# Kernel tuning notes

Hardware: AMD Instinct MI355X
Metric: run time of the kernel (lower is better)

## Reference

```python
import jax, jax.numpy as jnp
import numpy as np

N, NFEAT, NHID, NCLASS = 8192, 512, 256, 16
ALPHA = 0.01          # LeakyReLU negative slope
NEG = -9.0e15         # mask fill value from the original code
ADJ_DENSITY = 0.01    # ~82 neighbors per node


def setup_inputs() -> dict:
    key = jax.random.key(0)
    ks = jax.random.split(key, 9)
    x = jax.random.normal(ks[0], (N, NFEAT), jnp.float32)
    # sparse binary adjacency with self-loops, stored dense as in the torch code
    adj = (jax.random.uniform(ks[1], (N, N)) < ADJ_DENSITY).astype(jnp.int32)
    adj = adj.at[jnp.arange(N), jnp.arange(N)].set(1)
    s = 0.05
    W1 = jax.random.normal(ks[2], (NFEAT, NHID), jnp.float32) * s   # gc1.weight
    b1 = jax.random.normal(ks[3], (NHID,), jnp.float32) * s         # gc1.bias
    Wa = jax.random.normal(ks[4], (NHID, NHID), jnp.float32) * s    # out_att.W (nhid*nheads -> nhid)
    a_vec = jax.random.normal(ks[5], (2 * NHID, 1), jnp.float32) * s  # out_att.a
    W3 = jax.random.normal(ks[6], (NHID, NCLASS), jnp.float32) * s  # gc3.weight
    b3 = jax.random.normal(ks[7], (NCLASS,), jnp.float32) * s       # gc3.bias
    return {"x": x, "adj": adj, "W1": W1, "b1": b1, "Wa": Wa,
            "a_vec": a_vec, "W3": W3, "b3": b3}


def reference(x, adj, W1, b1, Wa, a_vec, W3, b3):
    adjf = adj.astype(x.dtype)
    # gc1: spmm(adj, x @ W1) + b1, then ReLU  (eval mode -> dropout is identity)
    h1 = jax.nn.relu(adjf @ (x @ W1) + b1)        # [N, NHID]
    feat = h1
    # out_att (GraphAttentionLayer, concat=False)
    Wh = h1 @ Wa                                   # [N, NHID]
    f1 = Wh @ a_vec[:NHID]                         # [N, 1]
    f2 = Wh @ a_vec[NHID:]                         # [N, 1]
    e = jax.nn.leaky_relu(f1 + f2.T, ALPHA)        # dense [N, N] scores
    e = jnp.where(adj > 0, e, jnp.asarray(NEG, x.dtype))
    attention = jax.nn.softmax(e, axis=1)          # row-wise masked softmax
    h_prime = attention @ Wh                       # [N, NHID]
    a_out = jax.nn.elu(h_prime)                    # x = F.elu(a)
    # gc3
    out = adjf @ (a_out @ W3) + b3                 # [N, NCLASS]
    return (jax.nn.sigmoid(out), attention, jnp.concatenate([feat, out], axis=1))
```

## Files before the change

kernel.cpp:

```cpp
#include <hip/hip_runtime.h>
#include <hip/hip_bf16.h>

#define NN    8192
#define NFEAT 512
#define NHID  256
#define NCLASS 16
#define ELLW  256

typedef __hip_bfloat16 bf16;
typedef unsigned short u16;
typedef __bf16 bf16x8 __attribute__((ext_vector_type(8)));
typedef float  f32x4  __attribute__((ext_vector_type(4)));
typedef int    i32x4  __attribute__((ext_vector_type(4)));

__global__ __launch_bounds__(256) void probe_dtype2(const u16* __restrict__ a, int na,
                                                    const u16* __restrict__ b, int nb,
                                                    int* __restrict__ cnt) {
  int c = 0;
  for (int i = blockIdx.x * 256 + threadIdx.x; i < na; i += gridDim.x * 256)
    if (((a[i] >> 7) & 0xFF) == 0xFF) c++;
  for (int i = blockIdx.x * 256 + threadIdx.x; i < nb; i += gridDim.x * 256)
    if (((b[i] >> 7) & 0xFF) == 0xFF) c++;
  if (c) atomicAdd(cnt, c);
}

__global__ __launch_bounds__(256) void convert_bf(const void* __restrict__ src,
                                                  bf16* __restrict__ dst, int n,
                                                  const int* __restrict__ flagcnt) {
  bool isf32 = (*flagcnt > 16);
  int i = blockIdx.x * 256 + threadIdx.x;
  if (i < n) {
    if (isf32) dst[i] = __float2bfloat16(((const float*)src)[i]);
    else       dst[i] = ((const bf16*)src)[i];
  }
}

__global__ __launch_bounds__(256) void convert_rest(const void* __restrict__ W1r,
                                                    const void* __restrict__ War,
                                                    const void* __restrict__ b1r,
                                                    const void* __restrict__ avr,
                                                    const void* __restrict__ W3r,
                                                    const void* __restrict__ b3r,
                                                    bf16* __restrict__ W1t,
                                                    bf16* __restrict__ Wat,
                                                    float* __restrict__ b1f,
                                                    float* __restrict__ avecf,
                                                    float* __restrict__ W3f,
                                                    float* __restrict__ b3f,
                                                    const int* __restrict__ flagcnt) {
  bool isf32 = (*flagcnt > 16);
  auto rd = [&](const void* p, int i) -> float {
    return isf32 ? ((const float*)p)[i] : __bfloat162float(((const bf16*)p)[i]);
  };
  const int n1 = NFEAT * NHID;
  const int n2 = n1 + NHID * NHID;
  const int n3 = n2 + NHID;
  const int n4 = n3 + 2 * NHID;
  const int n5 = n4 + NHID * NCLASS;
  const int n6 = n5 + NCLASS;
  for (int i = blockIdx.x * 256 + threadIdx.x; i < n6; i += gridDim.x * 256) {
    if (i < n1)      { int k = i / NHID, n = i % NHID; W1t[(size_t)n * NFEAT + k] = __float2bfloat16(rd(W1r, i)); }
    else if (i < n2) { int j = i - n1; int k = j / NHID, n = j % NHID; Wat[(size_t)n * NHID + k] = __float2bfloat16(rd(War, j)); }
    else if (i < n3) b1f[i - n2] = rd(b1r, i - n2);
    else if (i < n4) avecf[i - n3] = rd(avr, i - n3);
    else if (i < n5) W3f[i - n4] = rd(W3r, i - n4);
    else             b3f[i - n5] = rd(b3r, i - n5);
  }
}

__global__ __launch_bounds__(256) void build_ell(const int* __restrict__ adj,
                                                 int* __restrict__ ell_cnt,
                                                 u16* __restrict__ ell_col) {
  __shared__ int cnt;
  int row = blockIdx.x;
  if (threadIdx.x == 0) cnt = 0;
  __syncthreads();
  const i32x4* arow = (const i32x4*)(adj + (size_t)row * NN);
  u16* crow = ell_col + (size_t)row * ELLW;
  int lane = threadIdx.x & 63;
  unsigned long long lt = ((unsigned long long)1 << lane) - 1;
  for (int j4 = threadIdx.x; j4 < NN / 4; j4 += 256) {
    i32x4 v = __builtin_nontemporal_load(&arow[j4]);
    unsigned long long m0 = __ballot(v.x != 0);
    unsigned long long m1 = __ballot(v.y != 0);
    unsigned long long m2 = __ballot(v.z != 0);
    unsigned long long m3 = __ballot(v.w != 0);
    int c0 = __popcll(m0), c1 = __popcll(m1), c2 = __popcll(m2), c3 = __popcll(m3);
    int total = c0 + c1 + c2 + c3;
    int base = 0;
    if (lane == 0 && total) base = atomicAdd(&cnt, total);
    base = __shfl(base, 0, 64);
    int col = j4 * 4;
    if (v.x) { int p = base + __popcll(m0 & lt);                 if (p < ELLW) crow[p] = (u16)col;       }
    if (v.y) { int p = base + c0 + __popcll(m1 & lt);            if (p < ELLW) crow[p] = (u16)(col + 1); }
    if (v.z) { int p = base + c0 + c1 + __popcll(m2 & lt);       if (p < ELLW) crow[p] = (u16)(col + 2); }
    if (v.w) { int p = base + c0 + c1 + c2 + __popcll(m3 & lt);  if (p < ELLW) crow[p] = (u16)(col + 3); }
  }
  __syncthreads();
  if (threadIdx.x == 0) ell_cnt[row] = cnt < ELLW ? cnt : ELLW;
}

#define TM 64
#define TN 64
#define LDSP 72

__global__ __launch_bounds__(256) void gemm_bt(const bf16* __restrict__ A, int lda,
                                               const bf16* __restrict__ Bt, int ldb,
                                               bf16* __restrict__ C, int ldc, int K) {
  __shared__ __align__(16) bf16 sA[TM * LDSP];
  __shared__ __align__(16) bf16 sB[TN * LDSP];
  int bm = blockIdx.x, bn = blockIdx.y;
  int t = threadIdx.x;
  int wave = t >> 6, lane = t & 63;
  int quad = lane >> 4, l16 = lane & 15;
  f32x4 acc[4] = {};

  int srow = t >> 2;
  int sk   = (t & 3) * 16;
  const size_t abase = (size_t)(bm * TM + srow) * lda + sk;
  const size_t bbase = (size_t)(bn * TN + srow) * ldb + sk;

  uint4 pa0 = *(const uint4*)&A[abase];
  uint4 pa1 = *(const uint4*)&A[abase + 8];
  uint4 pb0 = *(const uint4*)&Bt[bbase];
  uint4 pb1 = *(const uint4*)&Bt[bbase + 8];

  for (int kt = 0; kt < K; kt += 64) {
    *(uint4*)&sA[srow * LDSP + sk]     = pa0;
    *(uint4*)&sA[srow * LDSP + sk + 8] = pa1;
    *(uint4*)&sB[srow * LDSP + sk]     = pb0;
    *(uint4*)&sB[srow * LDSP + sk + 8] = pb1;
    __syncthreads();
    if (kt + 64 < K) {
      pa0 = *(const uint4*)&A[abase + kt + 64];
      pa1 = *(const uint4*)&A[abase + kt + 72];
      pb0 = *(const uint4*)&Bt[bbase + kt + 64];
      pb1 = *(const uint4*)&Bt[bbase + kt + 72];
    }
    bf16x8 af0 = *(const bf16x8*)&sA[(wave * 16 + l16) * LDSP + quad * 8];
    bf16x8 af1 = *(const bf16x8*)&sA[(wave * 16 + l16) * LDSP + 32 + quad * 8];
#pragma unroll
    for (int c = 0; c < 4; ++c) {
      bf16x8 bf0 = *(const bf16x8*)&sB[(c * 16 + l16) * LDSP + quad * 8];
      bf16x8 bf1 = *(const bf16x8*)&sB[(c * 16 + l16) * LDSP + 32 + quad * 8];
      acc[c] = __builtin_amdgcn_mfma_f32_16x16x32_bf16(af0, bf0, acc[c], 0, 0, 0);
      acc[c] = __builtin_amdgcn_mfma_f32_16x16x32_bf16(af1, bf1, acc[c], 0, 0, 0);
    }
    __syncthreads();
  }
  int row0 = bm * TM + wave * 16 + quad * 4;
  int col0 = bn * TN;
#pragma unroll
  for (int c = 0; c < 4; ++c) {
#pragma unroll
    for (int r = 0; r < 4; ++r) {
      C[(size_t)(row0 + r) * ldc + col0 + c * 16 + l16] = __float2bfloat16(acc[c][r]);
    }
  }
}

__global__ __launch_bounds__(256) void spmm_h1(const bf16* __restrict__ XW,
                                               const int* __restrict__ ell_cnt,
                                               const u16* __restrict__ ell_col,
                                               const float* __restrict__ b1,
                                               float* __restrict__ out2,
                                               bf16* __restrict__ h1b) {
  __shared__ int sc0[ELLW], sc1[ELLW];
  int r0 = blockIdx.x * 2, r1 = r0 + 1;
  int t = threadIdx.x;
  int nn0 = ell_cnt[r0], nn1 = ell_cnt[r1];
  const u16* c0 = ell_col + (size_t)r0 * ELLW;
  const u16* c1 = ell_col + (size_t)r1 * ELLW;
  for (int k = t; k < nn0; k += 256) sc0[k] = c0[k];
  for (int k = t; k < nn1; k += 256) sc1[k] = c1[k];
  __syncthreads();
  float a0 = 0.f, a1 = 0.f;
#pragma unroll 4
  for (int k = 0; k < nn0; ++k) a0 += __bfloat162float(XW[(size_t)sc0[k] * NHID + t]);
#pragma unroll 4
  for (int k = 0; k < nn1; ++k) a1 += __bfloat162float(XW[(size_t)sc1[k] * NHID + t]);
  float bb = b1[t];
  a0 = fmaxf(a0 + bb, 0.f);
  a1 = fmaxf(a1 + bb, 0.f);
  out2[(size_t)r0 * (NHID + NCLASS) + t] = a0;
  out2[(size_t)r1 * (NHID + NCLASS) + t] = a1;
  h1b[(size_t)r0 * NHID + t] = __float2bfloat16(a0);
  h1b[(size_t)r1 * NHID + t] = __float2bfloat16(a1);
}

__global__ __launch_bounds__(256) void f12_kernel(const bf16* __restrict__ Wh,
                                                  const float* __restrict__ avec,
                                                  float* __restrict__ f12) {
  int wave = threadIdx.x >> 6, lane = threadIdx.x & 63;
  int row = blockIdx.x * 4 + wave;
  const bf16* wr = Wh + (size_t)row * NHID;
  float s1 = 0.f, s2 = 0.f;
  for (int k = lane; k < NHID; k += 64) {
    float w = __bfloat162float(wr[k]);
    s1 += w * avec[k];
    s2 += w * avec[NHID + k];
  }
  for (int o = 32; o > 0; o >>= 1) {
    s1 += __shfl_down(s1, o, 64);
    s2 += __shfl_down(s2, o, 64);
  }
  if (lane == 0) { f12[row] = s1; f12[NN + row] = s2; }
}

__global__ __launch_bounds__(256) void attn_fused(const bf16* __restrict__ Wh,
                                                  const int* __restrict__ ell_cnt,
                                                  const u16* __restrict__ ell_col,
                                                  const float* __restrict__ f12,
                                                  float* __restrict__ att,
                                                  bf16* __restrict__ aout) {
  __shared__ float p[ELLW];
  __shared__ int scols[ELLW];
  __shared__ float red[8];
  int row = blockIdx.x, t = threadIdx.x;
  int nn = ell_cnt[row];
  const u16* cr = ell_col + (size_t)row * ELLW;
  float f1i = f12[row];
  const float* f2 = f12 + NN;

  f32x4* dst = (f32x4*)(att + (size_t)row * NN);
  f32x4 z = {0.f, 0.f, 0.f, 0.f};
#pragma unroll
  for (int k = t; k < NN / 4; k += 256) __builtin_nontemporal_store(z, &dst[k]);

  for (int k = t; k < nn; k += 256) scols[k] = cr[k];
  __syncthreads();

  float lmax = -1e30f;
  for (int k = t; k < nn; k += 256) {
    float e = f1i + f2[scols[k]];
    e = (e > 0.f) ? e : 0.01f * e;
    p[k] = e;
    lmax = fmaxf(lmax, e);
  }
  for (int o = 32; o > 0; o >>= 1) lmax = fmaxf(lmax, __shfl_down(lmax, o, 64));
  if ((t & 63) == 0) red[t >> 6] = lmax;
  __syncthreads();
  float gmax = fmaxf(fmaxf(red[0], red[1]), fmaxf(red[2], red[3]));

  float lsum = 0.f;
  for (int k = t; k < nn; k += 256) {
    float ex = __expf(p[k] - gmax);
    p[k] = ex;
    lsum += ex;
  }
  for (int o = 32; o > 0; o >>= 1) lsum += __shfl_down(lsum, o, 64);
  __syncthreads();
  if ((t & 63) == 0) red[4 + (t >> 6)] = lsum;
  __syncthreads();
  float inv = 1.f / fmaxf(red[4] + red[5] + red[6] + red[7], 1e-30f);

  for (int k = t; k < nn; k += 256)
    att[(size_t)row * NN + scols[k]] = p[k] * inv;

  float acc = 0.f;
#pragma unroll 8
  for (int k = 0; k < nn; ++k)
    acc += p[k] * __bfloat162float(Wh[(size_t)scols[k] * NHID + t]);
  acc *= inv;
  float e = (acc > 0.f) ? acc : (__expf(acc) - 1.f);
  aout[(size_t)row * NHID + t] = __float2bfloat16(e);
}

__global__ __launch_bounds__(256) void attn_sparse(const bf16* __restrict__ Wh,
                                                   const int* __restrict__ ell_cnt,
                                                   const u16* __restrict__ ell_col,
                                                   const float* __restrict__ f12,
                                                   bf16* __restrict__ aout) {
  __shared__ float p[ELLW];
  __shared__ int scols[ELLW];
  __shared__ float red[8];
  int row = blockIdx.x, t = threadIdx.x;
  int nn = ell_cnt[row];
  const u16* cr = ell_col + (size_t)row * ELLW;
  float f1i = f12[row];
  const float* f2 = f12 + NN;
  for (int k = t; k < nn; k += 256) scols[k] = cr[k];
  __syncthreads();
  float lmax = -1e30f;
  for (int k = t; k < nn; k += 256) {
    float e = f1i + f2[scols[k]];
    e = (e > 0.f) ? e : 0.01f * e;
    p[k] = e;
    lmax = fmaxf(lmax, e);
  }
  for (int o = 32; o > 0; o >>= 1) lmax = fmaxf(lmax, __shfl_down(lmax, o, 64));
  if ((t & 63) == 0) red[t >> 6] = lmax;
  __syncthreads();
  float gmax = fmaxf(fmaxf(red[0], red[1]), fmaxf(red[2], red[3]));
  float lsum = 0.f;
  for (int k = t; k < nn; k += 256) {
    float ex = __expf(p[k] - gmax);
    p[k] = ex;
    lsum += ex;
  }
  for (int o = 32; o > 0; o >>= 1) lsum += __shfl_down(lsum, o, 64);
  __syncthreads();
  if ((t & 63) == 0) red[4 + (t >> 6)] = lsum;
  __syncthreads();
  float inv = 1.f / fmaxf(red[4] + red[5] + red[6] + red[7], 1e-30f);
  float acc = 0.f;
  for (int k = 0; k < nn; ++k)
    acc += p[k] * __bfloat162float(Wh[(size_t)scols[k] * NHID + t]);
  acc *= inv;
  float e = (acc > 0.f) ? acc : (__expf(acc) - 1.f);
  aout[(size_t)row * NHID + t] = __float2bfloat16(e);
}

__global__ __launch_bounds__(256) void attn_dense(const int* __restrict__ adj,
                                                  const float* __restrict__ f12,
                                                  float* __restrict__ att) {
  __shared__ __align__(16) float rowbuf[NN];
  __shared__ float se[ELLW];
  __shared__ int sj[ELLW];
  __shared__ float red[8];
  __shared__ int cnt;
  int row = blockIdx.x, t = threadIdx.x;
  if (t == 0) cnt = 0;
  f32x4* rb4 = (f32x4*)rowbuf;
  f32x4 z = {0.f, 0.f, 0.f, 0.f};
  for (int k = t; k < NN / 4; k += 256) rb4[k] = z;
  float f1i = f12[row];
  const float* f2 = f12 + NN;
  __syncthreads();
  const int4* arow = (const int4*)(adj + (size_t)row * NN);
  for (int j4 = t; j4 < NN / 4; j4 += 256) {
    int4 v = arow[j4];
    int base = j4 * 4;
    if (v.x) { int p = atomicAdd(&cnt, 1); if (p < ELLW) { sj[p] = base;     se[p] = f1i + f2[base];     } }
    if (v.y) { int p = atomicAdd(&cnt, 1); if (p < ELLW) { sj[p] = base + 1; se[p] = f1i + f2[base + 1]; } }
    if (v.z) { int p = atomicAdd(&cnt, 1); if (p < ELLW) { sj[p] = base + 2; se[p] = f1i + f2[base + 2]; } }
    if (v.w) { int p = atomicAdd(&cnt, 1); if (p < ELLW) { sj[p] = base + 3; se[p] = f1i + f2[base + 3]; } }
  }
  __syncthreads();
  int nn = cnt < ELLW ? cnt : ELLW;
  float lmax = -1e30f;
  for (int k = t; k < nn; k += 256) {
    float e = se[k];
    e = (e > 0.f) ? e : 0.01f * e;
    se[k] = e;
    lmax = fmaxf(lmax, e);
  }
  for (int o = 32; o > 0; o >>= 1) lmax = fmaxf(lmax, __shfl_down(lmax, o, 64));
  if ((t & 63) == 0) red[t >> 6] = lmax;
  __syncthreads();
  float gmax = fmaxf(fmaxf(red[0], red[1]), fmaxf(red[2], red[3]));
  float lsum = 0.f;
  for (int k = t; k < nn; k += 256) {
    float ex = __expf(se[k] - gmax);
    se[k] = ex;
    lsum += ex;
  }
  for (int o = 32; o > 0; o >>= 1) lsum += __shfl_down(lsum, o, 64);
  __syncthreads();
  if ((t & 63) == 0) red[4 + (t >> 6)] = lsum;
  __syncthreads();
  float inv = 1.f / fmaxf(red[4] + red[5] + red[6] + red[7], 1e-30f);
  for (int k = t; k < nn; k += 256) rowbuf[sj[k]] = se[k] * inv;
  __syncthreads();
  const f32x4* src = (const f32x4*)rowbuf;
  f32x4* dst = (f32x4*)(att + (size_t)row * NN);
  for (int k = t; k < NN / 4; k += 256) dst[k] = src[k];
}

__global__ __launch_bounds__(256) void gemm3(const bf16* __restrict__ aout,
                                             const float* __restrict__ W3,
                                             float* __restrict__ A3) {
  __shared__ float sW[NHID * NCLASS];
  __shared__ bf16 sa[16 * NHID];
  int t = threadIdx.x;
  for (int k = t; k < NHID * NCLASS; k += 256) sW[k] = W3[k];
  int r0 = blockIdx.x * 16;
  for (int k = t; k < 16 * NHID; k += 256) sa[k] = aout[(size_t)r0 * NHID + k];
  __syncthreads();
  int r = t >> 4, c = t & 15;
  float acc = 0.f;
#pragma unroll 8
  for (int k = 0; k < NHID; ++k)
    acc += __bfloat162float(sa[r * NHID + k]) * sW[k * NCLASS + c];
  A3[(size_t)(r0 + r) * NCLASS + c] = acc;
}

__global__ __launch_bounds__(256) void spmm_out2(const float* __restrict__ A3,
                                                 const int* __restrict__ ell_cnt,
                                                 const u16* __restrict__ ell_col,
                                                 const float* __restrict__ b3,
                                                 float* __restrict__ out2,
                                                 float* __restrict__ out0,
                                                 int write_sig) {
  int g = blockIdx.x * 256 + threadIdx.x;
  int row = g >> 4, c = g & 15;
  int nn = ell_cnt[row];
  const u16* cr = ell_col + (size_t)row * ELLW;
  float acc = b3[c];
#pragma unroll 8
  for (int k = 0; k < nn; ++k)
    acc += A3[(size_t)cr[k] * NCLASS + c];
  out2[(size_t)row * (NHID + NCLASS) + NHID + c] = acc;
  if (write_sig) out0[g] = 1.f / (1.f + __expf(-acc));
}

__global__ __launch_bounds__(256) void copy_f32(const float* __restrict__ src,
                                                float* __restrict__ dst, int n) {
  int i = blockIdx.x * 256 + threadIdx.x;
  if (i < n) dst[i] = src[i];
}

__global__ __launch_bounds__(256) void sigmoid_from_out2(const float* __restrict__ out2,
                                                         float* __restrict__ out0) {
  int g = blockIdx.x * 256 + threadIdx.x;
  int row = g >> 4, c = g & 15;
  float v = out2[(size_t)row * (NHID + NCLASS) + NHID + c];
  out0[g] = 1.f / (1.f + __expf(-v));
}

extern "C" void kernel_launch(void* const* d_in, const int* in_sizes, int n_in,
                              void* d_out, int out_size, void* d_ws, size_t ws_size,
                              hipStream_t stream) {
  const void* x_raw    = d_in[0];
  const int*  adj      = (const int*)d_in[1];
  const void* W1_raw   = d_in[2];
  const void* b1_raw   = d_in[3];
  const void* Wa_raw   = d_in[4];
  const void* avec_raw = d_in[5];
  const void* W3_raw   = d_in[6];
  const void* b3_raw   = d_in[7];

  float* out0 = (float*)d_out;
  float* out1 = out0 + (size_t)NN * NCLASS;
  float* out2 = out1 + (size_t)NN * NN;

  const size_t NEED = 36u << 20;
  bool useWS = (d_ws != nullptr) && (ws_size >= NEED);

  char* a = useWS ? (char*)d_ws : (char*)out1;
  size_t o = 0;
  auto carve = [&](size_t bytes) { char* p = a + o; o += (bytes + 4095) & ~(size_t)4095; return p; };
  int*   flag    = (int*)  carve(4096);
  int*   ell_cnt = (int*)  carve((size_t)NN * 4);
  u16*   ell_col = (u16*)  carve((size_t)NN * ELLW * 2);
  bf16*  xc      = (bf16*) carve((size_t)NN * NFEAT * 2);
  bf16*  W1t     = (bf16*) carve((size_t)NHID * NFEAT * 2);
  bf16*  Wat     = (bf16*) carve((size_t)NHID * NHID * 2);
  float* avecf   = (float*)carve((size_t)2 * NHID * 4);
  float* b1f     = (float*)carve((size_t)NHID * 4);
  float* b3f     = (float*)carve((size_t)NCLASS * 4);
  float* W3f     = (float*)carve((size_t)NHID * NCLASS * 4);
  bf16*  XW      = (bf16*) carve((size_t)NN * NHID * 2);
  bf16*  h1b     = (bf16*) carve((size_t)NN * NHID * 2);
  bf16*  Wh      = (bf16*) carve((size_t)NN * NHID * 2);
  float* f12a    = (float*)carve((size_t)2 * NN * 4);
  bf16*  aout    = (bf16*) carve((size_t)NN * NHID * 2);
  float* A3ws    = (float*)carve((size_t)NN * NCLASS * 4);

  float* A3 = useWS ? A3ws : out0;
  float* f12stash = out0;

  (void)hipMemsetAsync(flag, 0, 4, stream);
  probe_dtype2<<<128, 256, 0, stream>>>((const u16*)x_raw, NN * NFEAT,
                                        (const u16*)W1_raw, NFEAT * NHID, flag);
  convert_bf<<<(NN * NFEAT + 255) / 256, 256, 0, stream>>>(x_raw, xc, NN * NFEAT, flag);
  convert_rest<<<256, 256, 0, stream>>>(W1_raw, Wa_raw, b1_raw, avec_raw, W3_raw, b3_raw,
                                        W1t, Wat, b1f, avecf, W3f, b3f, flag);

  build_ell<<<NN, 256, 0, stream>>>(adj, ell_cnt, ell_col);
  gemm_bt<<<dim3(NN / TM, NHID / TN), 256, 0, stream>>>(xc, NFEAT, W1t, NFEAT, XW, NHID, NFEAT);
  spmm_h1<<<NN / 2, 256, 0, stream>>>(XW, ell_cnt, ell_col, b1f, out2, h1b);
  gemm_bt<<<dim3(NN / TM, NHID / TN), 256, 0, stream>>>(h1b, NHID, Wat, NHID, Wh, NHID, NHID);
  f12_kernel<<<NN / 4, 256, 0, stream>>>(Wh, avecf, f12a);

  if (useWS) {
    attn_fused<<<NN, 256, 0, stream>>>(Wh, ell_cnt, ell_col, f12a, out1, aout);
    gemm3<<<NN / 16, 256, 0, stream>>>(aout, W3f, A3);
    spmm_out2<<<NN * NCLASS / 256, 256, 0, stream>>>(A3, ell_cnt, ell_col, b3f, out2, out0, 1);
  } else {
    attn_sparse<<<NN, 256, 0, stream>>>(Wh, ell_cnt, ell_col, f12a, aout);
    gemm3<<<NN / 16, 256, 0, stream>>>(aout, W3f, A3);
    spmm_out2<<<NN * NCLASS / 256, 256, 0, stream>>>(A3, ell_cnt, ell_col, b3f, out2, out0, 0);
    copy_f32<<<(2 * NN + 255) / 256, 256, 0, stream>>>(f12a, f12stash, 2 * NN);
    attn_dense<<<NN, 256, 0, stream>>>(adj, f12stash, out1);
    sigmoid_from_out2<<<NN * NCLASS / 256, 256, 0, stream>>>(out2, out0);
  }
}
```

Measured before the change: 642.8 us.

## Merge conversion kernels, vectorize SpMM gathers, stage attention row in LDS

```diff
diff --git a/kernel.cpp b/kernel.cpp
--- a/kernel.cpp
+++ b/kernel.cpp
@@ -12,6 +12,14 @@
 typedef __bf16 bf16x8 __attribute__((ext_vector_type(8)));
 typedef float  f32x4  __attribute__((ext_vector_type(4)));
 typedef int    i32x4  __attribute__((ext_vector_type(4)));
+
+__device__ inline float bf2f(u16 u) { return __uint_as_float(((unsigned int)u) << 16); }
+__device__ inline u16 f2bfu(float f) {
+  bf16 b = __float2bfloat16(f);
+  u16 u;
+  __builtin_memcpy(&u, &b, 2);
+  return u;
+}
 
 __global__ __launch_bounds__(256) void probe_dtype2(const u16* __restrict__ a, int na,
                                                     const u16* __restrict__ b, int nb,
@@ -24,47 +32,52 @@
   if (c) atomicAdd(cnt, c);
 }
 
-__global__ __launch_bounds__(256) void convert_bf(const void* __restrict__ src,
-                                                  bf16* __restrict__ dst, int n,
-                                                  const int* __restrict__ flagcnt) {
-  bool isf32 = (*flagcnt > 16);
-  int i = blockIdx.x * 256 + threadIdx.x;
-  if (i < n) {
-    if (isf32) dst[i] = __float2bfloat16(((const float*)src)[i]);
-    else       dst[i] = ((const bf16*)src)[i];
-  }
-}
-
-__global__ __launch_bounds__(256) void convert_rest(const void* __restrict__ W1r,
-                                                    const void* __restrict__ War,
-                                                    const void* __restrict__ b1r,
-                                                    const void* __restrict__ avr,
-                                                    const void* __restrict__ W3r,
-                                                    const void* __restrict__ b3r,
-                                                    bf16* __restrict__ W1t,
-                                                    bf16* __restrict__ Wat,
-                                                    float* __restrict__ b1f,
-                                                    float* __restrict__ avecf,
-                                                    float* __restrict__ W3f,
-                                                    float* __restrict__ b3f,
-                                                    const int* __restrict__ flagcnt) {
+__global__ __launch_bounds__(256) void convert_all(const void* __restrict__ x_raw,
+                                                   const void* __restrict__ W1r,
+                                                   const void* __restrict__ War,
+                                                   const void* __restrict__ b1r,
+                                                   const void* __restrict__ avr,
+                                                   const void* __restrict__ W3r,
+                                                   const void* __restrict__ b3r,
+                                                   bf16* __restrict__ xc,
+                                                   bf16* __restrict__ W1t,
+                                                   bf16* __restrict__ Wat,
+                                                   float* __restrict__ b1f,
+                                                   float* __restrict__ avecf,
+                                                   float* __restrict__ W3f,
+                                                   float* __restrict__ b3f,
+                                                   const int* __restrict__ flagcnt) {
   bool isf32 = (*flagcnt > 16);
   auto rd = [&](const void* p, int i) -> float {
     return isf32 ? ((const float*)p)[i] : __bfloat162float(((const bf16*)p)[i]);
   };
+  const int n4x = NN * NFEAT / 4;
   const int n1 = NFEAT * NHID;
   const int n2 = n1 + NHID * NHID;
   const int n3 = n2 + NHID;
   const int n4 = n3 + 2 * NHID;
   const int n5 = n4 + NHID * NCLASS;
   const int n6 = n5 + NCLASS;
-  for (int i = blockIdx.x * 256 + threadIdx.x; i < n6; i += gridDim.x * 256) {
-    if (i < n1)      { int k = i / NHID, n = i % NHID; W1t[(size_t)n * NFEAT + k] = __float2bfloat16(rd(W1r, i)); }
-    else if (i < n2) { int j = i - n1; int k = j / NHID, n = j % NHID; Wat[(size_t)n * NHID + k] = __float2bfloat16(rd(War, j)); }
-    else if (i < n3) b1f[i - n2] = rd(b1r, i - n2);
-    else if (i < n4) avecf[i - n3] = rd(avr, i - n3);
-    else if (i < n5) W3f[i - n4] = rd(W3r, i - n4);
-    else             b3f[i - n5] = rd(b3r, i - n5);
+  const int total = n4x + n6;
+  for (int i = blockIdx.x * 256 + threadIdx.x; i < total; i += gridDim.x * 256) {
+    if (i < n4x) {
+      ushort4 o;
+      if (isf32) {
+        f32x4 v = ((const f32x4*)x_raw)[i];
+        o.x = f2bfu(v.x); o.y = f2bfu(v.y); o.z = f2bfu(v.z); o.w = f2bfu(v.w);
+      } else {
+        o = ((const ushort4*)x_raw)[i];
+      }
+      ((ushort4*)xc)[i] = o;
+    } else {
+      int j = i - n4x;
+      if (j < n1)      { int k = j / NHID, n = j % NHID; W1t[(size_t)n * NFEAT + k] = __float2bfloat16(rd(W1r, j)); }
+      else if (j < n2) { int q = j - n1; int k = q / NHID, n = q % NHID; Wat[(size_t)n * NHID + k] = __float2bfloat16(rd(War, q)); }
+      else if (j < n3) b1f[j - n2] = rd(b1r, j - n2);
+      else if (j < n4) avecf[j - n3] = rd(avr, j - n3);
+      else if (j < n5) W3f[j - n4] = rd(W3r, j - n4);
+      else             b3f[j - n5] = rd(b3r, j - n5);
+    }
   }
 }
 
@@ -165,27 +178,28 @@
                                                const float* __restrict__ b1,
                                                float* __restrict__ out2,
                                                bf16* __restrict__ h1b) {
-  __shared__ int sc0[ELLW], sc1[ELLW];
-  int r0 = blockIdx.x * 2, r1 = r0 + 1;
-  int t = threadIdx.x;
-  int nn0 = ell_cnt[r0], nn1 = ell_cnt[r1];
-  const u16* c0 = ell_col + (size_t)r0 * ELLW;
-  const u16* c1 = ell_col + (size_t)r1 * ELLW;
-  for (int k = t; k < nn0; k += 256) sc0[k] = c0[k];
-  for (int k = t; k < nn1; k += 256) sc1[k] = c1[k];
-  __syncthreads();
-  float a0 = 0.f, a1 = 0.f;
+  __shared__ int sc[4][ELLW];
+  int wave = threadIdx.x >> 6, lane = threadIdx.x & 63;
+  int row = blockIdx.x * 4 + wave;
+  int nn = ell_cnt[row];
+  const u16* cr = ell_col + (size_t)row * ELLW;
+  for (int k = lane; k < nn; k += 64) sc[wave][k] = cr[k];
+  float a0 = 0.f, a1 = 0.f, a2 = 0.f, a3 = 0.f;
+  const int c0 = lane * 4;
 #pragma unroll 4
-  for (int k = 0; k < nn0; ++k) a0 += __bfloat162float(XW[(size_t)sc0[k] * NHID + t]);
-#pragma unroll 4
-  for (int k = 0; k < nn1; ++k) a1 += __bfloat162float(XW[(size_t)sc1[k] * NHID + t]);
-  float bb = b1[t];
-  a0 = fmaxf(a0 + bb, 0.f);
-  a1 = fmaxf(a1 + bb, 0.f);
-  out2[(size_t)r0 * (NHID + NCLASS) + t] = a0;
-  out2[(size_t)r1 * (NHID + NCLASS) + t] = a1;
-  h1b[(size_t)r0 * NHID + t] = __float2bfloat16(a0);
-  h1b[(size_t)r1 * NHID + t] = __float2bfloat16(a1);
+  for (int k = 0; k < nn; ++k) {
+    ushort4 v = *(const ushort4*)&XW[(size_t)sc[wave][k] * NHID + c0];
+    a0 += bf2f(v.x); a1 += bf2f(v.y); a2 += bf2f(v.z); a3 += bf2f(v.w);
+  }
+  f32x4 bb = *(const f32x4*)&b1[c0];
+  a0 = fmaxf(a0 + bb.x, 0.f);
+  a1 = fmaxf(a1 + bb.y, 0.f);
+  a2 = fmaxf(a2 + bb.z, 0.f);
+  a3 = fmaxf(a3 + bb.w, 0.f);
+  f32x4 r; r.x = a0; r.y = a1; r.z = a2; r.w = a3;
+  *(f32x4*)&out2[(size_t)row * (NHID + NCLASS) + c0] = r;
+  ushort4 h; h.x = f2bfu(a0); h.y = f2bfu(a1); h.z = f2bfu(a2); h.w = f2bfu(a3);
+  *(ushort4*)&h1b[(size_t)row * NHID + c0] = h;
 }
 
 __global__ __launch_bounds__(256) void f12_kernel(const bf16* __restrict__ Wh,
@@ -213,20 +227,22 @@
                                                   const float* __restrict__ f12,
                                                   float* __restrict__ att,
                                                   bf16* __restrict__ aout) {
+  __shared__ __align__(16) float rowbuf[NN];
   __shared__ float p[ELLW];
   __shared__ int scols[ELLW];
   __shared__ float red[8];
+  __shared__ __align__(16) float hacc[4][NHID];
   int row = blockIdx.x, t = threadIdx.x;
+  int wave = t >> 6, lane = t & 63;
   int nn = ell_cnt[row];
   const u16* cr = ell_col + (size_t)row * ELLW;
   float f1i = f12[row];
   const float* f2 = f12 + NN;
 
-  f32x4* dst = (f32x4*)(att + (size_t)row * NN);
+  f32x4* rb4 = (f32x4*)rowbuf;
   f32x4 z = {0.f, 0.f, 0.f, 0.f};
 #pragma unroll
-  for (int k = t; k < NN / 4; k += 256) __builtin_nontemporal_store(z, &dst[k]);
-
+  for (int k = t; k < NN / 4; k += 256) rb4[k] = z;
   for (int k = t; k < nn; k += 256) scols[k] = cr[k];
   __syncthreads();
 
@@ -238,7 +254,7 @@
     lmax = fmaxf(lmax, e);
   }
   for (int o = 32; o > 0; o >>= 1) lmax = fmaxf(lmax, __shfl_down(lmax, o, 64));
-  if ((t & 63) == 0) red[t >> 6] = lmax;
+  if (lane == 0) red[wave] = lmax;
   __syncthreads();
   float gmax = fmaxf(fmaxf(red[0], red[1]), fmaxf(red[2], red[3]));
 
@@ -250,19 +266,33 @@
   }
   for (int o = 32; o > 0; o >>= 1) lsum += __shfl_down(lsum, o, 64);
   __syncthreads();
-  if ((t & 63) == 0) red[4 + (t >> 6)] = lsum;
+  if (lane == 0) red[4 + wave] = lsum;
   __syncthreads();
   float inv = 1.f / fmaxf(red[4] + red[5] + red[6] + red[7], 1e-30f);
 
-  for (int k = t; k < nn; k += 256)
-    att[(size_t)row * NN + scols[k]] = p[k] * inv;
-
-  float acc = 0.f;
-#pragma unroll 8
-  for (int k = 0; k < nn; ++k)
-    acc += p[k] * __bfloat162float(Wh[(size_t)scols[k] * NHID + t]);
-  acc *= inv;
-  float e = (acc > 0.f) ? acc : (__expf(acc) - 1.f);
+  for (int k = t; k < nn; k += 256) rowbuf[scols[k]] = p[k] * inv;
+
+  const int c0 = lane * 4;
+  float a0 = 0.f, a1 = 0.f, a2 = 0.f, a3 = 0.f;
+#pragma unroll 4
+  for (int k = wave; k < nn; k += 4) {
+    float pk = p[k];
+    ushort4 v = *(const ushort4*)&Wh[(size_t)scols[k] * NHID + c0];
+    a0 += pk * bf2f(v.x);
+    a1 += pk * bf2f(v.y);
+    a2 += pk * bf2f(v.z);
+    a3 += pk * bf2f(v.w);
+  }
+  f32x4 pa; pa.x = a0; pa.y = a1; pa.z = a2; pa.w = a3;
+  *(f32x4*)&hacc[wave][c0] = pa;
+  __syncthreads();
+
+  f32x4* dst = (f32x4*)(att + (size_t)row * NN);
+#pragma unroll
+  for (int k = t; k < NN / 4; k += 256) __builtin_nontemporal_store(rb4[k], &dst[k]);
+
+  float s = (hacc[0][t] + hacc[1][t] + hacc[2][t] + hacc[3][t]) * inv;
+  float e = (s > 0.f) ? s : (__expf(s) - 1.f);
   aout[(size_t)row * NHID + t] = __float2bfloat16(e);
 }
 
@@ -463,13 +493,12 @@
   (void)hipMemsetAsync(flag, 0, 4, stream);
   probe_dtype2<<<128, 256, 0, stream>>>((const u16*)x_raw, NN * NFEAT,
                                         (const u16*)W1_raw, NFEAT * NHID, flag);
-  convert_bf<<<(NN * NFEAT + 255) / 256, 256, 0, stream>>>(x_raw, xc, NN * NFEAT, flag);
-  convert_rest<<<256, 256, 0, stream>>>(W1_raw, Wa_raw, b1_raw, avec_raw, W3_raw, b3_raw,
-                                        W1t, Wat, b1f, avecf, W3f, b3f, flag);
+  convert_all<<<2048, 256, 0, stream>>>(x_raw, W1_raw, Wa_raw, b1_raw, avec_raw, W3_raw, b3_raw,
+                                        xc, W1t, Wat, b1f, avecf, W3f, b3f, flag);
 
   build_ell<<<NN, 256, 0, stream>>>(adj, ell_cnt, ell_col);
   gemm_bt<<<dim3(NN / TM, NHID / TN), 256, 0, stream>>>(xc, NFEAT, W1t, NFEAT, XW, NHID, NFEAT);
-  spmm_h1<<<NN / 2, 256, 0, stream>>>(XW, ell_cnt, ell_col, b1f, out2, h1b);
+  spmm_h1<<<NN / 4, 256, 0, stream>>>(XW, ell_cnt, ell_col, b1f, out2, h1b);
   gemm_bt<<<dim3(NN / TM, NHID / TN), 256, 0, stream>>>(h1b, NHID, Wat, NHID, Wh, NHID, NHID);
   f12_kernel<<<NN / 4, 256, 0, stream>>>(Wh, avecf, f12a);
 
```

Measured after the change: 575.5 us. -10.5%, faster.
